# Performance work log

Hardware: AMD Instinct MI355X
Metric: run time of the kernel (lower is better)

## Reference

```python
import jax, jax.numpy as jnp
import numpy as np

B, E, D, L, R = 32, 30000, 200, 50, 474
GAMMA, ALPHA, BETA = 9.0, 0.3, 0.7


def _gate(x_ent, x_lit, Wg, bg, W1, W2, gate_bias):
    # Gate module: x = [x_ent; x_lit]; out = (1-g)*x_ent + g*tanh(Linear(x))
    x = jnp.concatenate([x_ent, x_lit], axis=-1)
    g_emb = jnp.tanh(x @ Wg.T + bg)
    g = jax.nn.sigmoid(x_ent @ W1.T + x_lit @ W2.T + gate_bias)
    return (1.0 - g) * x_ent + g * g_emb


def setup_inputs() -> dict:
    key = jax.random.key(0)
    ks = jax.random.split(key, 11)
    rn = lambda k, shape: jax.random.normal(k, shape, jnp.float32) * 0.05
    return {
        'e1': jax.random.randint(ks[0], (B,), 0, E),
        'rel': jax.random.randint(ks[1], (B,), 0, R),
        'e2_multi': jax.random.randint(ks[2], (B, E), 0, 2).astype(jnp.int32),
        'emb_e': rn(ks[3], (E, D)),
        'emb_rel': rn(ks[4], (R, D)),
        'num_lit': jax.random.uniform(ks[5], (E, L), jnp.float32),
        'Wg': rn(ks[6], (D, D + L)),
        'bg': jnp.zeros((D,), jnp.float32),
        'W1': rn(ks[7], (D, D)),
        'W2': rn(ks[8], (D, L)),
        'gate_bias': jnp.zeros((D,), jnp.float32),
        'prob': jax.random.uniform(ks[9], (B, E), jnp.float32),
        'drop_mask': jax.random.randint(ks[10], (B, E), 0, 2).astype(jnp.float32),
    }


def reference(e1, rel, e2_multi, emb_e, emb_rel, num_lit, Wg, bg, W1, W2,
              gate_bias, prob, drop_mask):
    e2m = e2_multi.astype(emb_e.dtype)  # [B, E] multi-hot labels
    # literal-gated embeddings (inp_drop treated as eval/identity)
    e1_emb = _gate(emb_e[e1], num_lit[e1], Wg, bg, W1, W2, gate_bias)   # [B, D]
    e2_emb = _gate(emb_e, num_lit, Wg, bg, W1, W2, gate_bias)           # [E, D]
    rel_emb = emb_rel[rel]                                              # [B, D]

    # our_loss: weighted masked means over the full entity table
    e2p = e2m * prob                                                    # [B, E]
    pos_mean = (e2p @ e2_emb) / e2p.sum(-1, keepdims=True)              # [B, D]
    pos_mean = ALPHA * pos_mean + (1.0 - ALPHA) * e1_emb
    inv = 1.0 - e2m
    inv_drop = inv * drop_mask * 2.0  # F.dropout(p=0.5) = mask * 1/(1-p)
    neg_mean = (inv_drop @ e2_emb) / inv.sum(-1, keepdims=True)
    neg_mean = BETA * neg_mean + (1.0 - BETA) * e1_emb

    q = e1_emb + rel_emb                                                # [B, D]
    pos_s = jnp.abs(q - pos_mean).sum(-1, keepdims=True)                # [B, 1]
    neg_s = jnp.abs(q - neg_mean).sum(-1)                               # [B]
    # faithful to torch: [B] - [B,1] broadcasts to [B,B]
    loss = -jnp.mean(jax.nn.log_sigmoid(neg_s - pos_s))

    # broadcast L1 distance to ALL entities: [B, E, D] intermediate
    score = GAMMA - jnp.abs(q[:, None, :] - e2_emb[None, :, :]).sum(-1)  # [B, E]
    pred = jax.nn.sigmoid(score)
    return (pred, loss)
```

## Files before the change

kernel.cpp:

```cpp
#include <hip/hip_runtime.h>
#include <hip/hip_bf16.h>
#include <cstddef>

constexpr int B = 32, E = 30000, D = 200, L = 50;

using short8 = __attribute__((ext_vector_type(8))) short;
using f32x4  = __attribute__((ext_vector_type(4))) float;
using uint4v = __attribute__((ext_vector_type(4))) unsigned int;

__device__ __forceinline__ float sigmoidf_(float x){ return 1.f/(1.f+__expf(-x)); }
__device__ __forceinline__ float tanhf_(float x){
    float t = __expf(-2.f*fabsf(x));
    return copysignf((1.f-t)/(1.f+t), x);
}
__device__ __forceinline__ unsigned short f2bf(float x){
    unsigned u = __float_as_uint(x);
    u += 0x7fffu + ((u>>16)&1u);
    return (unsigned short)(u>>16);
}
__device__ __forceinline__ float bf2f(unsigned short h){
    return __uint_as_float(((unsigned)h)<<16);
}

__device__ __forceinline__ void split8(const float* v, short8& hv, short8& lv) {
    uint4v hp, lp;
    #pragma unroll
    for (int z = 0; z < 4; ++z) {
        unsigned u0 = __float_as_uint(v[2*z]), u1 = __float_as_uint(v[2*z+1]);
        hp[z] = __builtin_amdgcn_perm(u1, u0, 0x07060302u);
        float r0 = v[2*z]   - __uint_as_float(u0 & 0xFFFF0000u);
        float r1 = v[2*z+1] - __uint_as_float(u1 & 0xFFFF0000u);
        lp[z] = __builtin_amdgcn_perm(__float_as_uint(r1), __float_as_uint(r0), 0x07060302u);
    }
    hv = __builtin_bit_cast(short8, hp);
    lv = __builtin_bit_cast(short8, lp);
}

constexpr int WELEMS = 26*8*64*8;

__global__ __launch_bounds__(256) void wprep_kernel(
    const float* __restrict__ Wg, const float* __restrict__ W1,
    const float* __restrict__ W2,
    unsigned short* __restrict__ whi, unsigned short* __restrict__ wlo)
{
    int idx = blockIdx.x*256 + threadIdx.x;
    if (idx >= WELEMS) return;
    int j = idx & 7, l = (idx>>3)&63, ks = (idx>>9)&7, nt = idx>>12;
    int n = nt*16 + (l&15);
    int k = ks*32 + ((l>>4)&3)*8 + j;
    float v = 0.f;
    if (n < 208) {
        int d = n;
        if (d < 200 && k < 250) v = Wg[d*250 + k];
    } else {
        int d = n - 208;
        if (d < 200) {
            if (k < 200)      v = W1[d*200 + k];
            else if (k < 250) v = W2[d*50 + (k-200)];
        }
    }
    unsigned short h = f2bf(v);
    whi[idx] = h;
    wlo[idx] = f2bf(v - bf2f(h));
}

__global__ __launch_bounds__(256) void sums_kernel(
    const int* __restrict__ e2m, const float* __restrict__ prob,
    float* __restrict__ psum8, float* __restrict__ isum8)
{
    const int tid = threadIdx.x;
    const int b = blockIdx.x >> 3, ch = blockIdx.x & 7;
    const int es = ch * 3750;
    const int*   mrow = e2m  + (size_t)b * E + es;
    const float* prow = prob + (size_t)b * E + es;
    float sp = 0.f, si = 0.f;
    for (int i = tid; i < 3750; i += 256) {
        float m = (float)mrow[i];
        sp = fmaf(m, prow[i], sp);
        si += (1.f - m);
    }
    #pragma unroll
    for (int off = 32; off >= 1; off >>= 1) {
        sp += __shfl_down(sp, off);
        si += __shfl_down(si, off);
    }
    __shared__ float rp[4], ri[4];
    if ((tid & 63) == 0) { rp[tid >> 6] = sp; ri[tid >> 6] = si; }
    __syncthreads();
    if (tid == 0) {
        psum8[b*8 + ch] = rp[0] + rp[1] + rp[2] + rp[3];
        isum8[b*8 + ch] = ri[0] + ri[1] + ri[2] + ri[3];
    }
}

__global__ __launch_bounds__(512) void gate_kernel(
    const float* __restrict__ emb_e, const float* __restrict__ num_lit,
    const unsigned short* __restrict__ whi, const unsigned short* __restrict__ wlo,
    const float* __restrict__ bg, const float* __restrict__ gbias,
    float* __restrict__ e2_emb)
{
    __shared__ __align__(16) float PW[4*7*64*4];

    const int tid  = threadIdx.x;
    const int lane = tid & 63;
    const int wid  = tid >> 6;
    const int mt   = wid & 3;
    const int g    = wid >> 2;
    const int mb   = blockIdx.x >> 1;
    const int h    = blockIdx.x & 1;
    const int e0   = mb * 64;
    const int start = h * 6;
    const int ntb  = start + g * 13;

    const int arow = e0 + mt*16 + (lane & 15);
    const int kgrp = ((lane >> 4) & 3) * 8;
    const bool rok = arow < E;
    const float* aeb = emb_e   + (size_t)arow * 200;
    const float* alb = num_lit + (size_t)arow * 50;

    f32x4 acc[7];
    #pragma unroll
    for (int i = 0; i < 7; ++i) acc[i] = (f32x4){0.f,0.f,0.f,0.f};

#define WOFF(p, ks) (((size_t)(((ntb + (p))*8 + c*2 + (ks))*64 + lane))*8)

    for (int c = 0; c < 4; ++c) {
        short8 xh[2], xl[2];
        #pragma unroll
        for (int ks = 0; ks < 2; ++ks) {
            const int k0 = c*64 + ks*32 + kgrp;
            float v[8];
            if (rok && k0 <= 192) {
                float4 f0 = *(const float4*)(aeb + k0);
                float4 f1 = *(const float4*)(aeb + k0 + 4);
                v[0]=f0.x; v[1]=f0.y; v[2]=f0.z; v[3]=f0.w;
                v[4]=f1.x; v[5]=f1.y; v[6]=f1.z; v[7]=f1.w;
            } else if (rok && k0 <= 240) {
                const int kl = k0 - 200;
                #pragma unroll
                for (int z = 0; z < 4; ++z) {
                    float2 f = *(const float2*)(alb + kl + 2*z);
                    v[2*z] = f.x; v[2*z+1] = f.y;
                }
            } else if (rok && k0 == 248) {
                float2 f = *(const float2*)(alb + 48);
                v[0] = f.x; v[1] = f.y;
                #pragma unroll
                for (int z = 2; z < 8; ++z) v[z] = 0.f;
            } else {
                #pragma unroll
                for (int z = 0; z < 8; ++z) v[z] = 0.f;
            }
            split8(v, xh[ks], xl[ks]);
        }

        short8 pwh[2][2], pwl[2][2];
        pwh[0][0] = *(const short8*)(whi + WOFF(0,0));
        pwh[0][1] = *(const short8*)(whi + WOFF(0,1));
        pwl[0][0] = *(const short8*)(wlo + WOFF(0,0));
        pwl[0][1] = *(const short8*)(wlo + WOFF(0,1));

        #pragma unroll
        for (int p = 0; p < 7; ++p) {
            const int cur = p & 1, nxt = cur ^ 1;
            if (p < 6) {
                pwh[nxt][0] = *(const short8*)(whi + WOFF(p+1,0));
                pwh[nxt][1] = *(const short8*)(whi + WOFF(p+1,1));
                pwl[nxt][0] = *(const short8*)(wlo + WOFF(p+1,0));
                pwl[nxt][1] = *(const short8*)(wlo + WOFF(p+1,1));
            }
            #pragma unroll
            for (int ks = 0; ks < 2; ++ks) {
                acc[p] = __builtin_amdgcn_mfma_f32_16x16x32_bf16(xh[ks], pwh[cur][ks], acc[p], 0,0,0);
                acc[p] = __builtin_amdgcn_mfma_f32_16x16x32_bf16(xl[ks], pwh[cur][ks], acc[p], 0,0,0);
                acc[p] = __builtin_amdgcn_mfma_f32_16x16x32_bf16(xh[ks], pwl[cur][ks], acc[p], 0,0,0);
            }
        }
    }
#undef WOFF

    if (g == 1) {
        #pragma unroll
        for (int p = 0; p < 7; ++p)
            *(f32x4*)&PW[((mt*7 + p)*64 + lane)*4] = acc[p];
    }
    __syncthreads();
    if (g == 0) {
        const int col = lane & 15, rg = lane >> 4;
        #pragma unroll
        for (int p = 0; p < 7; ++p) {
            int d = (start + p)*16 + col;
            if (d >= 200) continue;
            float bgd = bg[d], gbd = gbias[d];
            f32x4 p2 = *(const f32x4*)&PW[((mt*7 + p)*64 + lane)*4];
            #pragma unroll
            for (int r = 0; r < 4; ++r) {
                int e = e0 + mt*16 + rg*4 + r;
                if (e >= E) continue;
                float pre1 = acc[p][r] + bgd;
                float pre2 = p2[r] + gbd;
                float gt = sigmoidf_(pre2);
                float t  = tanhf_(pre1);
                float emb = emb_e[(size_t)e*200 + d];
                e2_emb[(size_t)e*200 + d] = (1.f - gt)*emb + gt*t;
            }
        }
    }
}

__global__ __launch_bounds__(256) void q_kernel(
    const int* __restrict__ e1, const int* __restrict__ rel,
    const float* __restrict__ emb_rel, const float* __restrict__ e2_emb,
    float* __restrict__ q)
{
    int tid = threadIdx.x;
    for (int idx = tid; idx < B * D; idx += 256) {
        int b = idx / D, d = idx % D;
        q[idx] = e2_emb[(size_t)e1[b] * D + d] + emb_rel[(size_t)rel[b] * D + d];
    }
}

constexpr int GVB = 235;

__global__ __launch_bounds__(256) void gemv_kernel(
    const int* __restrict__ e2m, const float* __restrict__ prob,
    const float* __restrict__ drop, const float* __restrict__ e2_emb,
    float* __restrict__ gpart)
{
    __shared__ unsigned short Bf[13312];
    __shared__ unsigned short Acp[2048], Acn[2048];
    const int tid = threadIdx.x, lane = tid & 63, w = tid >> 6;
    const int e0 = blockIdx.x * 128;

    f32x4 acc[2][2][4];
    #pragma unroll
    for (int a = 0; a < 2; ++a)
        #pragma unroll
        for (int m = 0; m < 2; ++m)
            #pragma unroll
            for (int s = 0; s < 4; ++s) acc[a][m][s] = (f32x4){0.f,0.f,0.f,0.f};

    for (int c = 0; c < 2; ++c) {
        const int ec = e0 + c*64;
        if (c) __syncthreads();

        {
            const int bb = tid >> 3, part = tid & 7;
            const int eb = ec + part*8;
            float cp[8], cn[8];
            size_t base = (size_t)bb * E + eb;
            if (eb + 7 < E) {
                int4   m0 = *(const int4*)(e2m + base),   m1 = *(const int4*)(e2m + base + 4);
                float4 p0 = *(const float4*)(prob + base), p1 = *(const float4*)(prob + base + 4);
                float4 d0 = *(const float4*)(drop + base), d1 = *(const float4*)(drop + base + 4);
                cp[0]=m0.x?p0.x:0.f; cn[0]=m0.x?0.f:2.f*d0.x;
                cp[1]=m0.y?p0.y:0.f; cn[1]=m0.y?0.f:2.f*d0.y;
                cp[2]=m0.z?p0.z:0.f; cn[2]=m0.z?0.f:2.f*d0.z;
                cp[3]=m0.w?p0.w:0.f; cn[3]=m0.w?0.f:2.f*d0.w;
                cp[4]=m1.x?p1.x:0.f; cn[4]=m1.x?0.f:2.f*d1.x;
                cp[5]=m1.y?p1.y:0.f; cn[5]=m1.y?0.f:2.f*d1.y;
                cp[6]=m1.z?p1.z:0.f; cn[6]=m1.z?0.f:2.f*d1.z;
                cp[7]=m1.w?p1.w:0.f; cn[7]=m1.w?0.f:2.f*d1.w;
            } else {
                #pragma unroll
                for (int j = 0; j < 8; ++j) {
                    int e = eb + j;
                    cp[j] = 0.f; cn[j] = 0.f;
                    if (e < E) {
                        int m = e2m[base + j];
                        cp[j] = m ? prob[base + j] : 0.f;
                        cn[j] = m ? 0.f : 2.f * drop[base + j];
                    }
                }
            }
            short8 scp, scn;
            #pragma unroll
            for (int j = 0; j < 8; ++j) { scp[j] = (short)f2bf(cp[j]); scn[j] = (short)f2bf(cn[j]); }
            int off = (((bb >> 4)*2 + (part >> 2))*64 + ((bb & 15) | ((part & 3) << 4)))*8;
            *(short8*)&Acp[off] = scp;
            *(short8*)&Acn[off] = scn;
        }

        for (int s = tid; s < 3328; s += 256) {
            int el = s / 52, d4 = (s - el*52)*4;
            int e = ec + el;
            float4 f = make_float4(0.f,0.f,0.f,0.f);
            if (e < E && d4 < 200) f = *(const float4*)(e2_emb + (size_t)e*200 + d4);
            int ks = el >> 5, lp = (el >> 3) & 3, j = el & 7;
            float fv[4] = {f.x, f.y, f.z, f.w};
            #pragma unroll
            for (int z = 0; z < 4; ++z) {
                int d = d4 + z;
                Bf[(((d >> 4)*2 + ks)*64 + ((d & 15) | (lp << 4)))*8 + j] = f2bf(fv[z]);
            }
        }
        __syncthreads();

        short8 cpA[2][2], cnA[2][2];
        #pragma unroll
        for (int mtb = 0; mtb < 2; ++mtb)
            #pragma unroll
            for (int ks = 0; ks < 2; ++ks) {
                int fo = ((mtb*2 + ks)*64 + lane)*8;
                cpA[mtb][ks] = *(const short8*)&Acp[fo];
                cnA[mtb][ks] = *(const short8*)&Acn[fo];
            }
        #pragma unroll
        for (int ks = 0; ks < 2; ++ks)
            #pragma unroll
            for (int slot = 0; slot < 4; ++slot) {
                int nt = w + slot*4;
                if (nt < 13) {
                    short8 bf = *(const short8*)&Bf[((nt*2 + ks)*64 + lane)*8];
                    acc[0][0][slot] = __builtin_amdgcn_mfma_f32_16x16x32_bf16(cpA[0][ks], bf, acc[0][0][slot], 0,0,0);
                    acc[0][1][slot] = __builtin_amdgcn_mfma_f32_16x16x32_bf16(cpA[1][ks], bf, acc[0][1][slot], 0,0,0);
                    acc[1][0][slot] = __builtin_amdgcn_mfma_f32_16x16x32_bf16(cnA[0][ks], bf, acc[1][0][slot], 0,0,0);
                    acc[1][1][slot] = __builtin_amdgcn_mfma_f32_16x16x32_bf16(cnA[1][ks], bf, acc[1][1][slot], 0,0,0);
                }
            }
    }

    const int col = lane & 15, rg = lane >> 4;
    #pragma unroll
    for (int mat = 0; mat < 2; ++mat)
        #pragma unroll
        for (int mtb = 0; mtb < 2; ++mtb)
            #pragma unroll
            for (int slot = 0; slot < 4; ++slot) {
                int nt = w + slot*4;
                if (nt >= 13) continue;
                int d = nt*16 + col;
                if (d >= 200) continue;
                #pragma unroll
                for (int r = 0; r < 4; ++r) {
                    int b = mtb*16 + rg*4 + r;
                    gpart[(((size_t)blockIdx.x*2 + mat)*32 + b)*200 + d]
                        = acc[mat][mtb][slot][r];
                }
            }
}

__global__ __launch_bounds__(128) void gred_kernel(
    const float* __restrict__ gpart, float* __restrict__ posv, float* __restrict__ negv)
{
    int o = blockIdx.x*128 + threadIdx.x;
    float sp = 0.f, sn = 0.f;
    #pragma unroll 4
    for (int blk = 0; blk < GVB; ++blk) {
        sp += gpart[((size_t)blk*2 + 0)*6400 + o];
        sn += gpart[((size_t)blk*2 + 1)*6400 + o];
    }
    posv[o] = sp;
    negv[o] = sn;
}

__global__ __launch_bounds__(512) void score_kernel(
    const float* __restrict__ q, const float* __restrict__ e2_emb,
    float* __restrict__ pred)
{
    __shared__ __align__(16) float Es[64*204];
    const int tid = threadIdx.x, lane = tid & 63, w = tid >> 6;
    const int e0 = blockIdx.x * 64;

    for (int s = tid; s < 64*50; s += 512) {
        int er = s / 50, d4 = (s - er*50)*4;
        int e = e0 + er;
        float4 f = make_float4(0.f,0.f,0.f,0.f);
        if (e < E) f = *(const float4*)(e2_emb + (size_t)e*200 + d4);
        *(float4*)&Es[er*204 + d4] = f;
    }
    __syncthreads();

    const int b0 = w * 4;
    const float* erow = &Es[lane*204];
    float acc[4] = {0.f,0.f,0.f,0.f};
    #pragma unroll 5
    for (int dc = 0; dc < 200; dc += 8) {
        float4 ea = *(const float4*)(erow + dc);
        float4 eb = *(const float4*)(erow + dc + 4);
        #pragma unroll
        for (int i = 0; i < 4; ++i) {
            float4 qa = *(const float4*)(q + (b0+i)*200 + dc);
            float4 qb = *(const float4*)(q + (b0+i)*200 + dc + 4);
            acc[i] += fabsf(qa.x-ea.x) + fabsf(qa.y-ea.y) + fabsf(qa.z-ea.z) + fabsf(qa.w-ea.w)
                    + fabsf(qb.x-eb.x) + fabsf(qb.y-eb.y) + fabsf(qb.z-eb.z) + fabsf(qb.w-eb.w);
        }
    }
    int e = e0 + lane;
    if (e < E) {
        #pragma unroll
        for (int i = 0; i < 4; ++i)
            pred[(size_t)(b0+i)*E + e] = sigmoidf_(9.0f - acc[i]);
    }
}

__global__ __launch_bounds__(256) void final_kernel(
    const int* __restrict__ e1, const float* __restrict__ q,
    const float* __restrict__ posv, const float* __restrict__ negv,
    const float* __restrict__ psum8, const float* __restrict__ isum8,
    const float* __restrict__ e2_emb, float* __restrict__ loss_out)
{
    const int tid = threadIdx.x;
    __shared__ float SP[32], SI[32];
    if (tid < 32) {
        float s = 0.f, t = 0.f;
        #pragma unroll
        for (int k = 0; k < 8; ++k) { s += psum8[tid*8 + k]; t += isum8[tid*8 + k]; }
        SP[tid] = s; SI[tid] = t;
    }
    __syncthreads();

    const int b = tid >> 3, dl = tid & 7;
    const int e1b = e1[b];
    const float isp = 1.f / SP[b];
    const float isn = 1.f / SI[b];
    float ps = 0.f, ns = 0.f;
    #pragma unroll
    for (int t = 0; t < 25; ++t) {
        int d = dl*25 + t;
        float e1e = e2_emb[(size_t)e1b*200 + d];
        float pm = 0.3f * (posv[b*200 + d] * isp) + 0.7f * e1e;
        float nm = 0.7f * (negv[b*200 + d] * isn) + 0.3f * e1e;
        float qv = q[b*200 + d];
        ps += fabsf(qv - pm);
        ns += fabsf(qv - nm);
    }
    ps += __shfl_down(ps, 4, 8); ps += __shfl_down(ps, 2, 8); ps += __shfl_down(ps, 1, 8);
    ns += __shfl_down(ns, 4, 8); ns += __shfl_down(ns, 2, 8); ns += __shfl_down(ns, 1, 8);

    __shared__ float PS[B], NS[B];
    if (dl == 0) { PS[b] = ps; NS[b] = ns; }
    __syncthreads();

    float part = 0.f;
    #pragma unroll
    for (int r = 0; r < 4; ++r) {
        int idx = tid + r*256;
        int i = idx >> 5, j = idx & 31;
        float x = NS[j] - PS[i];
        part += fminf(x, 0.f) - log1pf(expf(-fabsf(x)));
    }
    #pragma unroll
    for (int off = 32; off >= 1; off >>= 1) part += __shfl_down(part, off);
    __shared__ float wr[4];
    if ((tid & 63) == 0) wr[tid >> 6] = part;
    __syncthreads();
    if (tid == 0) loss_out[0] = -(wr[0] + wr[1] + wr[2] + wr[3]) * (1.f/1024.f);
}

extern "C" void kernel_launch(void* const* d_in, const int* in_sizes, int n_in,
                              void* d_out, int out_size, void* d_ws, size_t ws_size,
                              hipStream_t stream)
{
    const int*   e1      = (const int*)d_in[0];
    const int*   rel     = (const int*)d_in[1];
    const int*   e2m     = (const int*)d_in[2];
    const float* emb_e   = (const float*)d_in[3];
    const float* emb_rel = (const float*)d_in[4];
    const float* num_lit = (const float*)d_in[5];
    const float* Wg      = (const float*)d_in[6];
    const float* bg      = (const float*)d_in[7];
    const float* W1      = (const float*)d_in[8];
    const float* W2      = (const float*)d_in[9];
    const float* gbias   = (const float*)d_in[10];
    const float* prob    = (const float*)d_in[11];
    const float* drop    = (const float*)d_in[12];

    float* pred = (float*)d_out;
    float* ws   = (float*)d_ws;

    float*          e2_emb = ws;
    float*          q      = ws + 6000000;
    unsigned short* whi    = (unsigned short*)(ws + 6006400);
    unsigned short* wlo    = (unsigned short*)(ws + 6059648);
    float*          gpart  = ws + 6112896;
    float*          posv   = ws + 9120896;
    float*          negv   = ws + 9127296;
    float*          psum8  = ws + 9133696;
    float*          isum8  = ws + 9133952;

    wprep_kernel<<<WELEMS/256, 256, 0, stream>>>(Wg, W1, W2, whi, wlo);
    sums_kernel<<<256, 256, 0, stream>>>(e2m, prob, psum8, isum8);
    gate_kernel<<<944, 512, 0, stream>>>(emb_e, num_lit, whi, wlo, bg, gbias, e2_emb);
    q_kernel<<<1, 256, 0, stream>>>(e1, rel, emb_rel, e2_emb, q);
    gemv_kernel<<<GVB, 256, 0, stream>>>(e2m, prob, drop, e2_emb, gpart);
    gred_kernel<<<50, 128, 0, stream>>>(gpart, posv, negv);
    score_kernel<<<(E + 63)/64, 512, 0, stream>>>(q, e2_emb, pred);
    final_kernel<<<1, 256, 0, stream>>>(e1, q, posv, negv, psum8, isum8, e2_emb,
                                        pred + (size_t)B*E);
}
```

Measured before the change: 272.4 us.

## Merge prep kernels, enlarge gate and gemv tiles, parallelize q kernel

Fuses the weight-prep and row-sum kernels into one launch. The gate kernel now handles 256 entities per block, with each wave doing four M-tiles so every weight fragment loaded is reused across them. The gemv kernel also takes 256 entities per block, which halves the partial buffers that the reduction has to sum. The q kernel is spread over 32 blocks. The costs are much higher register pressure in gate (28 accumulators per lane) and far fewer blocks (236 gate, 118 gemv), which may leave the GPU's compute units underused.

Result: slower. 292.6 us (+7.4%).

```diff
diff --git a/kernel.cpp b/kernel.cpp
--- a/kernel.cpp
+++ b/kernel.cpp
@@ -38,58 +38,58 @@
 
 constexpr int WELEMS = 26*8*64*8;
 
-__global__ __launch_bounds__(256) void wprep_kernel(
+__global__ __launch_bounds__(256) void prep_kernel(
     const float* __restrict__ Wg, const float* __restrict__ W1,
     const float* __restrict__ W2,
-    unsigned short* __restrict__ whi, unsigned short* __restrict__ wlo)
-{
-    int idx = blockIdx.x*256 + threadIdx.x;
-    if (idx >= WELEMS) return;
-    int j = idx & 7, l = (idx>>3)&63, ks = (idx>>9)&7, nt = idx>>12;
-    int n = nt*16 + (l&15);
-    int k = ks*32 + ((l>>4)&3)*8 + j;
-    float v = 0.f;
-    if (n < 208) {
-        int d = n;
-        if (d < 200 && k < 250) v = Wg[d*250 + k];
-    } else {
-        int d = n - 208;
-        if (d < 200) {
-            if (k < 200)      v = W1[d*200 + k];
-            else if (k < 250) v = W2[d*50 + (k-200)];
-        }
-    }
-    unsigned short h = f2bf(v);
-    whi[idx] = h;
-    wlo[idx] = f2bf(v - bf2f(h));
-}
-
-__global__ __launch_bounds__(256) void sums_kernel(
+    unsigned short* __restrict__ whi, unsigned short* __restrict__ wlo,
     const int* __restrict__ e2m, const float* __restrict__ prob,
     float* __restrict__ psum8, float* __restrict__ isum8)
 {
     const int tid = threadIdx.x;
-    const int b = blockIdx.x >> 3, ch = blockIdx.x & 7;
-    const int es = ch * 3750;
-    const int*   mrow = e2m  + (size_t)b * E + es;
-    const float* prow = prob + (size_t)b * E + es;
-    float sp = 0.f, si = 0.f;
-    for (int i = tid; i < 3750; i += 256) {
-        float m = (float)mrow[i];
-        sp = fmaf(m, prow[i], sp);
-        si += (1.f - m);
-    }
-    #pragma unroll
-    for (int off = 32; off >= 1; off >>= 1) {
-        sp += __shfl_down(sp, off);
-        si += __shfl_down(si, off);
-    }
-    __shared__ float rp[4], ri[4];
-    if ((tid & 63) == 0) { rp[tid >> 6] = sp; ri[tid >> 6] = si; }
-    __syncthreads();
-    if (tid == 0) {
-        psum8[b*8 + ch] = rp[0] + rp[1] + rp[2] + rp[3];
-        isum8[b*8 + ch] = ri[0] + ri[1] + ri[2] + ri[3];
+    if (blockIdx.x < 416) {
+        int idx = blockIdx.x*256 + tid;
+        if (idx >= WELEMS) return;
+        int j = idx & 7, l = (idx>>3)&63, ks = (idx>>9)&7, nt = idx>>12;
+        int n = nt*16 + (l&15);
+        int k = ks*32 + ((l>>4)&3)*8 + j;
+        float v = 0.f;
+        if (n < 208) {
+            int d = n;
+            if (d < 200 && k < 250) v = Wg[d*250 + k];
+        } else {
+            int d = n - 208;
+            if (d < 200) {
+                if (k < 200)      v = W1[d*200 + k];
+                else if (k < 250) v = W2[d*50 + (k-200)];
+            }
+        }
+        unsigned short h = f2bf(v);
+        whi[idx] = h;
+        wlo[idx] = f2bf(v - bf2f(h));
+    } else {
+        const int bid = blockIdx.x - 416;
+        const int b = bid >> 3, ch = bid & 7;
+        const int es = ch * 3750;
+        const int*   mrow = e2m  + (size_t)b * E + es;
+        const float* prow = prob + (size_t)b * E + es;
+        float sp = 0.f, si = 0.f;
+        for (int i = tid; i < 3750; i += 256) {
+            float m = (float)mrow[i];
+            sp = fmaf(m, prow[i], sp);
+            si += (1.f - m);
+        }
+        #pragma unroll
+        for (int off = 32; off >= 1; off >>= 1) {
+            sp += __shfl_down(sp, off);
+            si += __shfl_down(si, off);
+        }
+        __shared__ float rp[4], ri[4];
+        if ((tid & 63) == 0) { rp[tid >> 6] = sp; ri[tid >> 6] = si; }
+        __syncthreads();
+        if (tid == 0) {
+            psum8[b*8 + ch] = rp[0] + rp[1] + rp[2] + rp[3];
+            isum8[b*8 + ch] = ri[0] + ri[1] + ri[2] + ri[3];
+        }
     }
 }
 
@@ -104,54 +104,60 @@
     const int tid  = threadIdx.x;
     const int lane = tid & 63;
     const int wid  = tid >> 6;
-    const int mt   = wid & 3;
-    const int g    = wid >> 2;
+    const int g    = wid & 1;
+    const int rg   = wid >> 1;
     const int mb   = blockIdx.x >> 1;
     const int h    = blockIdx.x & 1;
-    const int e0   = mb * 64;
+    const int e0   = mb * 256;
     const int start = h * 6;
-    const int ntb  = start + g * 13;
-
-    const int arow = e0 + mt*16 + (lane & 15);
+    const int ntb  = g*13 + start;
+
+    const int rowbase = e0 + rg*64;
     const int kgrp = ((lane >> 4) & 3) * 8;
-    const bool rok = arow < E;
-    const float* aeb = emb_e   + (size_t)arow * 200;
-    const float* alb = num_lit + (size_t)arow * 50;
-
-    f32x4 acc[7];
-    #pragma unroll
-    for (int i = 0; i < 7; ++i) acc[i] = (f32x4){0.f,0.f,0.f,0.f};
+
+    f32x4 acc[7][4];
+    #pragma unroll
+    for (int p = 0; p < 7; ++p)
+        #pragma unroll
+        for (int m = 0; m < 4; ++m) acc[p][m] = (f32x4){0.f,0.f,0.f,0.f};
 
 #define WOFF(p, ks) (((size_t)(((ntb + (p))*8 + c*2 + (ks))*64 + lane))*8)
 
     for (int c = 0; c < 4; ++c) {
-        short8 xh[2], xl[2];
-        #pragma unroll
-        for (int ks = 0; ks < 2; ++ks) {
-            const int k0 = c*64 + ks*32 + kgrp;
-            float v[8];
-            if (rok && k0 <= 192) {
-                float4 f0 = *(const float4*)(aeb + k0);
-                float4 f1 = *(const float4*)(aeb + k0 + 4);
-                v[0]=f0.x; v[1]=f0.y; v[2]=f0.z; v[3]=f0.w;
-                v[4]=f1.x; v[5]=f1.y; v[6]=f1.z; v[7]=f1.w;
-            } else if (rok && k0 <= 240) {
-                const int kl = k0 - 200;
-                #pragma unroll
-                for (int z = 0; z < 4; ++z) {
-                    float2 f = *(const float2*)(alb + kl + 2*z);
-                    v[2*z] = f.x; v[2*z+1] = f.y;
+        short8 xh[4][2], xl[4][2];
+        #pragma unroll
+        for (int mt = 0; mt < 4; ++mt) {
+            const int arow = rowbase + mt*16 + (lane & 15);
+            const bool rok = arow < E;
+            const float* aeb = emb_e   + (size_t)arow * 200;
+            const float* alb = num_lit + (size_t)arow * 50;
+            #pragma unroll
+            for (int ks = 0; ks < 2; ++ks) {
+                const int k0 = c*64 + ks*32 + kgrp;
+                float v[8];
+                if (rok && k0 <= 192) {
+                    float4 f0 = *(const float4*)(aeb + k0);
+                    float4 f1 = *(const float4*)(aeb + k0 + 4);
+                    v[0]=f0.x; v[1]=f0.y; v[2]=f0.z; v[3]=f0.w;
+                    v[4]=f1.x; v[5]=f1.y; v[6]=f1.z; v[7]=f1.w;
+                } else if (rok && k0 <= 240) {
+                    const int kl = k0 - 200;
+                    #pragma unroll
+                    for (int z = 0; z < 4; ++z) {
+                        float2 f = *(const float2*)(alb + kl + 2*z);
+                        v[2*z] = f.x; v[2*z+1] = f.y;
+                    }
+                } else if (rok && k0 == 248) {
+                    float2 f = *(const float2*)(alb + 48);
+                    v[0] = f.x; v[1] = f.y;
+                    #pragma unroll
+                    for (int z = 2; z < 8; ++z) v[z] = 0.f;
+                } else {
+                    #pragma unroll
+                    for (int z = 0; z < 8; ++z) v[z] = 0.f;
                 }
-            } else if (rok && k0 == 248) {
-                float2 f = *(const float2*)(alb + 48);
-                v[0] = f.x; v[1] = f.y;
-                #pragma unroll
-                for (int z = 2; z < 8; ++z) v[z] = 0.f;
-            } else {
-                #pragma unroll
-                for (int z = 0; z < 8; ++z) v[z] = 0.f;
-            }
-            split8(v, xh[ks], xl[ks]);
+                split8(v, xh[mt][ks], xl[mt][ks]);
+            }
         }
 
         short8 pwh[2][2], pwl[2][2];
@@ -171,38 +177,44 @@
             }
             #pragma unroll
             for (int ks = 0; ks < 2; ++ks) {
-                acc[p] = __builtin_amdgcn_mfma_f32_16x16x32_bf16(xh[ks], pwh[cur][ks], acc[p], 0,0,0);
-                acc[p] = __builtin_amdgcn_mfma_f32_16x16x32_bf16(xl[ks], pwh[cur][ks], acc[p], 0,0,0);
-                acc[p] = __builtin_amdgcn_mfma_f32_16x16x32_bf16(xh[ks], pwl[cur][ks], acc[p], 0,0,0);
+                #pragma unroll
+                for (int mt = 0; mt < 4; ++mt) {
+                    acc[p][mt] = __builtin_amdgcn_mfma_f32_16x16x32_bf16(xh[mt][ks], pwh[cur][ks], acc[p][mt], 0,0,0);
+                    acc[p][mt] = __builtin_amdgcn_mfma_f32_16x16x32_bf16(xl[mt][ks], pwh[cur][ks], acc[p][mt], 0,0,0);
+                    acc[p][mt] = __builtin_amdgcn_mfma_f32_16x16x32_bf16(xh[mt][ks], pwl[cur][ks], acc[p][mt], 0,0,0);
+                }
             }
         }
     }
 #undef WOFF
 
-    if (g == 1) {
-        #pragma unroll
-        for (int p = 0; p < 7; ++p)
-            *(f32x4*)&PW[((mt*7 + p)*64 + lane)*4] = acc[p];
-    }
-    __syncthreads();
-    if (g == 0) {
-        const int col = lane & 15, rg = lane >> 4;
-        #pragma unroll
-        for (int p = 0; p < 7; ++p) {
-            int d = (start + p)*16 + col;
-            if (d >= 200) continue;
-            float bgd = bg[d], gbd = gbias[d];
-            f32x4 p2 = *(const f32x4*)&PW[((mt*7 + p)*64 + lane)*4];
-            #pragma unroll
-            for (int r = 0; r < 4; ++r) {
-                int e = e0 + mt*16 + rg*4 + r;
-                if (e >= E) continue;
-                float pre1 = acc[p][r] + bgd;
-                float pre2 = p2[r] + gbd;
-                float gt = sigmoidf_(pre2);
-                float t  = tanhf_(pre1);
-                float emb = emb_e[(size_t)e*200 + d];
-                e2_emb[(size_t)e*200 + d] = (1.f - gt)*emb + gt*t;
+    const int col = lane & 15, rgl = lane >> 4;
+    for (int mtp = 0; mtp < 4; ++mtp) {
+        if (mtp) __syncthreads();
+        if (g == 1) {
+            #pragma unroll
+            for (int p = 0; p < 7; ++p)
+                *(f32x4*)&PW[((rg*7 + p)*64 + lane)*4] = acc[p][mtp];
+        }
+        __syncthreads();
+        if (g == 0) {
+            #pragma unroll
+            for (int p = 0; p < 7; ++p) {
+                int d = (start + p)*16 + col;
+                if (d >= 200) continue;
+                float bgd = bg[d], gbd = gbias[d];
+                f32x4 p2 = *(const f32x4*)&PW[((rg*7 + p)*64 + lane)*4];
+                #pragma unroll
+                for (int r = 0; r < 4; ++r) {
+                    int e = rowbase + mtp*16 + rgl*4 + r;
+                    if (e >= E) continue;
+                    float pre1 = acc[p][mtp][r] + bgd;
+                    float pre2 = p2[r] + gbd;
+                    float gt = sigmoidf_(pre2);
+                    float t  = tanhf_(pre1);
+                    float emb = emb_e[(size_t)e*200 + d];
+                    e2_emb[(size_t)e*200 + d] = (1.f - gt)*emb + gt*t;
+                }
             }
         }
     }
@@ -213,14 +225,12 @@
     const float* __restrict__ emb_rel, const float* __restrict__ e2_emb,
     float* __restrict__ q)
 {
-    int tid = threadIdx.x;
-    for (int idx = tid; idx < B * D; idx += 256) {
-        int b = idx / D, d = idx % D;
-        q[idx] = e2_emb[(size_t)e1[b] * D + d] + emb_rel[(size_t)rel[b] * D + d];
-    }
-}
-
-constexpr int GVB = 235;
+    const int b = blockIdx.x, d = threadIdx.x;
+    if (d < 200)
+        q[b*200 + d] = e2_emb[(size_t)e1[b]*200 + d] + emb_rel[(size_t)rel[b]*200 + d];
+}
+
+constexpr int GVB = 118;
 
 __global__ __launch_bounds__(256) void gemv_kernel(
     const int* __restrict__ e2m, const float* __restrict__ prob,
@@ -230,7 +240,7 @@
     __shared__ unsigned short Bf[13312];
     __shared__ unsigned short Acp[2048], Acn[2048];
     const int tid = threadIdx.x, lane = tid & 63, w = tid >> 6;
-    const int e0 = blockIdx.x * 128;
+    const int e0 = blockIdx.x * 256;
 
     f32x4 acc[2][2][4];
     #pragma unroll
@@ -240,7 +250,7 @@
             #pragma unroll
             for (int s = 0; s < 4; ++s) acc[a][m][s] = (f32x4){0.f,0.f,0.f,0.f};
 
-    for (int c = 0; c < 2; ++c) {
+    for (int c = 0; c < 4; ++c) {
         const int ec = e0 + c*64;
         if (c) __syncthreads();
 
@@ -345,7 +355,7 @@
 {
     int o = blockIdx.x*128 + threadIdx.x;
     float sp = 0.f, sn = 0.f;
-    #pragma unroll 4
+    #pragma unroll 2
     for (int blk = 0; blk < GVB; ++blk) {
         sp += gpart[((size_t)blk*2 + 0)*6400 + o];
         sn += gpart[((size_t)blk*2 + 1)*6400 + o];
@@ -474,15 +484,15 @@
     unsigned short* whi    = (unsigned short*)(ws + 6006400);
     unsigned short* wlo    = (unsigned short*)(ws + 6059648);
     float*          gpart  = ws + 6112896;
-    float*          posv   = ws + 9120896;
-    float*          negv   = ws + 9127296;
-    float*          psum8  = ws + 9133696;
-    float*          isum8  = ws + 9133952;
-
-    wprep_kernel<<<WELEMS/256, 256, 0, stream>>>(Wg, W1, W2, whi, wlo);
-    sums_kernel<<<256, 256, 0, stream>>>(e2m, prob, psum8, isum8);
-    gate_kernel<<<944, 512, 0, stream>>>(emb_e, num_lit, whi, wlo, bg, gbias, e2_emb);
-    q_kernel<<<1, 256, 0, stream>>>(e1, rel, emb_rel, e2_emb, q);
+    float*          posv   = ws + 7623296;
+    float*          negv   = ws + 7629696;
+    float*          psum8  = ws + 7636096;
+    float*          isum8  = ws + 7636352;
+
+    prep_kernel<<<672, 256, 0, stream>>>(Wg, W1, W2, whi, wlo,
+                                         e2m, prob, psum8, isum8);
+    gate_kernel<<<236, 512, 0, stream>>>(emb_e, num_lit, whi, wlo, bg, gbias, e2_emb);
+    q_kernel<<<32, 256, 0, stream>>>(e1, rel, emb_rel, e2_emb, q);
     gemv_kernel<<<GVB, 256, 0, stream>>>(e2m, prob, drop, e2_emb, gpart);
     gred_kernel<<<50, 128, 0, stream>>>(gpart, posv, negv);
     score_kernel<<<(E + 63)/64, 512, 0, stream>>>(q, e2_emb, pred);
```
